# Kernel tuning notes

Hardware: AMD Instinct MI355X
Metric: run time of the kernel (lower is better)

The kernel has to match this reference:

```python
import jax, jax.numpy as jnp
import numpy as np

N_E, E_DIM, BETA = 1024, 64, 0.25

def setup_inputs() -> dict:
    key = jax.random.key(0)
    k1, k2 = jax.random.split(key)
    z = jax.random.normal(k1, (16, 4096, E_DIM), dtype=jnp.float32)
    embedding = jax.random.uniform(k2, (N_E, E_DIM), dtype=jnp.float32,
                                   minval=-1.0 / 256, maxval=1.0 / 256)
    return {"z": z, "embedding": embedding}

def reference(z, embedding):
    # z: [B, S, D]; embedding: [n_e, D]
    zf = z.reshape(-1, E_DIM)  # [N, D]
    # squared euclidean distances: ||z||^2 + ||e||^2 - 2 z e^T -> [N, n_e]
    d = (jnp.sum(zf * zf, axis=1, keepdims=True)
         + jnp.sum(embedding * embedding, axis=1)
         - 2.0 * jnp.matmul(zf, embedding.T))
    min_encoding_indices = jnp.argmin(d, axis=1)  # [N]
    z_q = embedding[min_encoding_indices].reshape(z.shape)  # [B, S, D]
    sg = jax.lax.stop_gradient
    loss = (jnp.mean((z_q - sg(z)) ** 2)
            + BETA * jnp.mean((sg(z_q) - z) ** 2))
    z_q = z + sg(z_q - z)  # straight-through estimator
    return (loss, z_q, min_encoding_indices)
```

## Files before the change

kernel.cpp:

```cpp
#include <hip/hip_runtime.h>


#define D 64
#define NE 1024
#define ROWS 64
#define TCODES 64
#define NTILES 16
#define TPB 256
#define ZSTR 64

#define SWZ(row, c) (((row) << 6) + ((((c) ^ ((row) & 7))) << 2))

__global__ __launch_bounds__(64, 4) void ee_kernel(const float* __restrict__ emb,
                                                   float* __restrict__ ee_ws) {
    const int j = blockIdx.x * 64 + threadIdx.x;
    {
#pragma clang fp contract(off)
        const float4* e4 = (const float4*)(emb + ((size_t)j << 6));
        float4 a = e4[0], b = e4[1];
        float r[8];
        r[0]=a.x*a.x; r[1]=a.y*a.y; r[2]=a.z*a.z; r[3]=a.w*a.w;
        r[4]=b.x*b.x; r[5]=b.y*b.y; r[6]=b.z*b.z; r[7]=b.w*b.w;
#pragma unroll
        for (int g = 1; g < 8; ++g) {
            float4 c = e4[2*g], e = e4[2*g + 1];
            r[0]=r[0]+c.x*c.x; r[1]=r[1]+c.y*c.y;
            r[2]=r[2]+c.z*c.z; r[3]=r[3]+c.w*c.w;
            r[4]=r[4]+e.x*e.x; r[5]=r[5]+e.y*e.y;
            r[6]=r[6]+e.z*e.z; r[7]=r[7]+e.w*e.w;
        }
        ee_ws[j] = ((r[0]+r[1])+(r[2]+r[3])) + ((r[4]+r[5])+(r[6]+r[7]));
    }
}

__global__ __launch_bounds__(TPB, 3) void vq_kernel(const float* __restrict__ z,
                                                    const float* __restrict__ emb,
                                                    const float* __restrict__ ee_ws,
                                                    float* __restrict__ out_loss,
                                                    float* __restrict__ out_zq,
                                                    float* __restrict__ out_idx,
                                                    float loss_scale) {
    __shared__ __align__(16) float z_lds[ROWS * ZSTR];
    __shared__ __align__(16) float e_lds[TCODES * ZSTR];
    __shared__ float ee_lds[NE];
    __shared__ float zz_lds[ROWS];
    __shared__ float smv[2 * ROWS];
    __shared__ int   smi[2 * ROWS];

    const int tid  = threadIdx.x;
    const int lane = tid & 63;
    const int w    = tid >> 6;
    const int rh   = w & 1;
    const int ch   = w >> 1;
    const int i8   = lane & 7;
    const int jg   = lane >> 3;
    const size_t blockRow = (size_t)blockIdx.x * ROWS;
    const int zrow0 = (rh << 5) + i8;

    {
        const float4* zg4 = (const float4*)(z + blockRow * D);
#pragma unroll
        for (int it = 0; it < 4; ++it) {
            int idx = tid + it * TPB;
            float4 v = zg4[idx];
            *(float4*)&z_lds[SWZ(idx >> 4, idx & 15)] = v;
        }
    }
    {
        float4 v = ((const float4*)ee_ws)[tid];
        *(float4*)&ee_lds[tid * 4] = v;
    }
    float4 pe0, pe1, pe2, pe3;
    {
        const float4* eg4 = (const float4*)emb;
        pe0 = eg4[tid];       pe1 = eg4[tid + 256];
        pe2 = eg4[tid + 512]; pe3 = eg4[tid + 768];
    }
    __syncthreads();

    if (tid < ROWS) {
        float zr[D];
#pragma unroll
        for (int c = 0; c < 16; ++c) {
            float4 v = *(const float4*)&z_lds[SWZ(tid, c)];
            zr[4*c+0]=v.x; zr[4*c+1]=v.y; zr[4*c+2]=v.z; zr[4*c+3]=v.w;
        }
        {
#pragma clang fp contract(off)
            float r[8];
#pragma unroll
            for (int jj = 0; jj < 8; ++jj) { float t = zr[jj]*zr[jj]; r[jj] = t; }
#pragma unroll
            for (int i = 8; i < 64; i += 8) {
#pragma unroll
                for (int jj = 0; jj < 8; ++jj) { float t = zr[i+jj]*zr[i+jj]; r[jj] = r[jj] + t; }
            }
            zz_lds[tid] = ((r[0]+r[1])+(r[2]+r[3])) + ((r[4]+r[5])+(r[6]+r[7]));
        }
    }

    float rb[4];  int rbj[4];
#pragma unroll
    for (int rr = 0; rr < 4; ++rr) { rb[rr] = __builtin_inff(); rbj[rr] = 0; }

    for (int t = 0; t < NTILES; ++t) {
        *(float4*)&e_lds[SWZ((tid      ) >> 4, (tid      ) & 15)] = pe0;
        *(float4*)&e_lds[SWZ((tid + 256) >> 4, (tid + 256) & 15)] = pe1;
        *(float4*)&e_lds[SWZ((tid + 512) >> 4, (tid + 512) & 15)] = pe2;
        *(float4*)&e_lds[SWZ((tid + 768) >> 4, (tid + 768) & 15)] = pe3;
        __syncthreads();

        if (t < NTILES - 1) {
            const float4* eg4 = (const float4*)(emb + (size_t)(t + 1) * TCODES * D);
            pe0 = eg4[tid];       pe1 = eg4[tid + 256];
            pe2 = eg4[tid + 512]; pe3 = eg4[tid + 768];
        }

        float4 acc[4][4];
#pragma unroll
        for (int rr = 0; rr < 4; ++rr)
#pragma unroll
            for (int cc = 0; cc < 4; ++cc)
                acc[rr][cc] = make_float4(0.f, 0.f, 0.f, 0.f);

#pragma unroll 2
        for (int c = 0; c < 16; ++c) {
            float4 zf[4], ef[4];
#pragma unroll
            for (int rr = 0; rr < 4; ++rr)
                zf[rr] = *(const float4*)&z_lds[SWZ(zrow0 + 8*rr, c)];
#pragma unroll
            for (int cc = 0; cc < 4; ++cc)
                ef[cc] = *(const float4*)&e_lds[SWZ((ch << 5) + jg + (cc << 3), c)];
#pragma unroll
            for (int rr = 0; rr < 4; ++rr)
#pragma unroll
                for (int cc = 0; cc < 4; ++cc) {
                    acc[rr][cc].x = fmaf(zf[rr].x, ef[cc].x, acc[rr][cc].x);
                    acc[rr][cc].y = fmaf(zf[rr].y, ef[cc].y, acc[rr][cc].y);
                    acc[rr][cc].z = fmaf(zf[rr].z, ef[cc].z, acc[rr][cc].z);
                    acc[rr][cc].w = fmaf(zf[rr].w, ef[cc].w, acc[rr][cc].w);
                }
        }

        const int cbase = t * TCODES + (ch << 5) + jg;
        const float ee0 = ee_lds[cbase];
        const float ee1 = ee_lds[cbase + 8];
        const float ee2 = ee_lds[cbase + 16];
        const float ee3 = ee_lds[cbase + 24];
#pragma unroll
        for (int rr = 0; rr < 4; ++rr) {
            const float zzv = zz_lds[zrow0 + 8*rr];
            float dot0 = (acc[rr][0].x + acc[rr][0].y) + (acc[rr][0].z + acc[rr][0].w);
            float dot1 = (acc[rr][1].x + acc[rr][1].y) + (acc[rr][1].z + acc[rr][1].w);
            float dot2 = (acc[rr][2].x + acc[rr][2].y) + (acc[rr][2].z + acc[rr][2].w);
            float dot3 = (acc[rr][3].x + acc[rr][3].y) + (acc[rr][3].z + acc[rr][3].w);
            float d0 = fmaf(-2.0f, dot0, zzv + ee0);
            float d1 = fmaf(-2.0f, dot1, zzv + ee1);
            float d2 = fmaf(-2.0f, dot2, zzv + ee2);
            float d3 = fmaf(-2.0f, dot3, zzv + ee3);
            float cv = d0; int cj = cbase;
            if (d1 < cv) { cv = d1; cj = cbase + 8;  }
            if (d2 < cv) { cv = d2; cj = cbase + 16; }
            if (d3 < cv) { cv = d3; cj = cbase + 24; }
            if (cv < rb[rr]) { rb[rr] = cv; rbj[rr] = cj; }
        }
        __syncthreads();
    }

#pragma unroll
    for (int rr = 0; rr < 4; ++rr) {
        float bv = rb[rr]; int bj = rbj[rr];
#pragma unroll
        for (int off = 8; off <= 32; off <<= 1) {
            float ov = __shfl_xor(bv, off);
            int   oi = __shfl_xor(bj, off);
            if (ov < bv || (ov == bv && oi < bj)) { bv = ov; bj = oi; }
        }
        if (jg == 0) {
            smv[ch * ROWS + zrow0 + 8*rr] = bv;
            smi[ch * ROWS + zrow0 + 8*rr] = bj;
        }
    }
    __syncthreads();

    const int erow = tid & 63;
    const int eg   = tid >> 6;

    float best = smv[erow]; int bi = smi[erow];
    {
        float v  = smv[ROWS + erow];
        int   ii = smi[ROWS + erow];
        if (v < best || (v == best && ii < bi)) { best = v; bi = ii; }
    }

    const float4* qe4 = (const float4*)(emb + ((size_t)bi << 6));
    float s = 0.f;
    float* orow = out_zq + (blockRow + erow) * D;
#pragma unroll
    for (int c = 0; c < 16; ++c) {
        float4 q  = qe4[c];
        float4 zv = *(const float4*)&z_lds[SWZ(erow, c)];
        float d0 = q.x - zv.x, d1 = q.y - zv.y, d2 = q.z - zv.z, d3 = q.w - zv.w;
        s += d0*d0; s += d1*d1; s += d2*d2; s += d3*d3;
        if ((c >> 2) == eg) {
            orow[4*c+0] = zv.x + d0; orow[4*c+1] = zv.y + d1;
            orow[4*c+2] = zv.z + d2; orow[4*c+3] = zv.w + d3;
        }
    }

    if (eg == 0) {
        out_idx[blockRow + erow] = (float)bi;
#pragma unroll
        for (int off = 32; off; off >>= 1) s += __shfl_down(s, off);
        if (tid == 0) atomicAdd(out_loss, s * loss_scale);
    }
}

extern "C" void kernel_launch(void* const* d_in, const int* in_sizes, int n_in,
                              void* d_out, int out_size, void* d_ws, size_t ws_size,
                              hipStream_t stream) {
    const float* z   = (const float*)d_in[0];
    const float* emb = (const float*)d_in[1];
    const int nz = in_sizes[0];
    const int N  = nz / D;

    float* out      = (float*)d_out;
    float* out_zq   = out + 1;
    float* out_idx  = out + 1 + (size_t)nz;
    float* ee_ws    = (float*)d_ws;

    const float loss_scale = 1.25f / (float)nz;

    hipMemsetAsync(out, 0, sizeof(float), stream);
    ee_kernel<<<NE / 64, 64, 0, stream>>>(emb, ee_ws);
    vq_kernel<<<N / ROWS, TPB, 0, stream>>>(z, emb, ee_ws, out, out_zq, out_idx,
                                            loss_scale);
}
```

Measured before the change: 217.0 us.

## Double codebook tile to 128 codes and give each wave all 64 rows

Codebook tiles grow from 64 to 128 codes, so the tile loop runs 8 times instead of 16 with half as many barriers. Each wave now covers all 64 z rows against its own 32 codes, so per-thread accumulators go from 16 to 32 float4 and every loaded code vector is reused across twice as many rows. The cross-wave argmin reduction widens from 2 to 4 partials. The cost is much higher register pressure (launch bounds lowered to 2 blocks per CU), a larger LDS footprint and twice the prefetch registers, all of which reduce occupancy.

```diff
diff --git a/kernel.cpp b/kernel.cpp
--- a/kernel.cpp
+++ b/kernel.cpp
@@ -4,8 +4,8 @@
 #define D 64
 #define NE 1024
 #define ROWS 64
-#define TCODES 64
-#define NTILES 16
+#define TCODES 128
+#define NTILES 8
 #define TPB 256
 #define ZSTR 64
 
@@ -33,7 +33,7 @@
     }
 }
 
-__global__ __launch_bounds__(TPB, 3) void vq_kernel(const float* __restrict__ z,
+__global__ __launch_bounds__(TPB, 2) void vq_kernel(const float* __restrict__ z,
                                                     const float* __restrict__ emb,
                                                     const float* __restrict__ ee_ws,
                                                     float* __restrict__ out_loss,
@@ -44,18 +44,15 @@
     __shared__ __align__(16) float e_lds[TCODES * ZSTR];
     __shared__ float ee_lds[NE];
     __shared__ float zz_lds[ROWS];
-    __shared__ float smv[2 * ROWS];
-    __shared__ int   smi[2 * ROWS];
+    __shared__ float smv[4 * ROWS];
+    __shared__ int   smi[4 * ROWS];
 
     const int tid  = threadIdx.x;
     const int lane = tid & 63;
     const int w    = tid >> 6;
-    const int rh   = w & 1;
-    const int ch   = w >> 1;
     const int i8   = lane & 7;
     const int jg   = lane >> 3;
     const size_t blockRow = (size_t)blockIdx.x * ROWS;
-    const int zrow0 = (rh << 5) + i8;
 
     {
         const float4* zg4 = (const float4*)(z + blockRow * D);
@@ -70,11 +67,13 @@
         float4 v = ((const float4*)ee_ws)[tid];
         *(float4*)&ee_lds[tid * 4] = v;
     }
-    float4 pe0, pe1, pe2, pe3;
+    float4 pe0, pe1, pe2, pe3, pe4, pe5, pe6, pe7;
     {
         const float4* eg4 = (const float4*)emb;
-        pe0 = eg4[tid];       pe1 = eg4[tid + 256];
-        pe2 = eg4[tid + 512]; pe3 = eg4[tid + 768];
+        pe0 = eg4[tid];        pe1 = eg4[tid + 256];
+        pe2 = eg4[tid + 512];  pe3 = eg4[tid + 768];
+        pe4 = eg4[tid + 1024]; pe5 = eg4[tid + 1280];
+        pe6 = eg4[tid + 1536]; pe7 = eg4[tid + 1792];
     }
     __syncthreads();
 
@@ -99,41 +98,47 @@
         }
     }
 
-    float rb[4];  int rbj[4];
-#pragma unroll
-    for (int rr = 0; rr < 4; ++rr) { rb[rr] = __builtin_inff(); rbj[rr] = 0; }
+    float rb[8];  int rbj[8];
+#pragma unroll
+    for (int rr = 0; rr < 8; ++rr) { rb[rr] = __builtin_inff(); rbj[rr] = 0; }
 
     for (int t = 0; t < NTILES; ++t) {
-        *(float4*)&e_lds[SWZ((tid      ) >> 4, (tid      ) & 15)] = pe0;
-        *(float4*)&e_lds[SWZ((tid + 256) >> 4, (tid + 256) & 15)] = pe1;
-        *(float4*)&e_lds[SWZ((tid + 512) >> 4, (tid + 512) & 15)] = pe2;
-        *(float4*)&e_lds[SWZ((tid + 768) >> 4, (tid + 768) & 15)] = pe3;
+        *(float4*)&e_lds[SWZ((tid       ) >> 4, (tid       ) & 15)] = pe0;
+        *(float4*)&e_lds[SWZ((tid +  256) >> 4, (tid +  256) & 15)] = pe1;
+        *(float4*)&e_lds[SWZ((tid +  512) >> 4, (tid +  512) & 15)] = pe2;
+        *(float4*)&e_lds[SWZ((tid +  768) >> 4, (tid +  768) & 15)] = pe3;
+        *(float4*)&e_lds[SWZ((tid + 1024) >> 4, (tid + 1024) & 15)] = pe4;
+        *(float4*)&e_lds[SWZ((tid + 1280) >> 4, (tid + 1280) & 15)] = pe5;
+        *(float4*)&e_lds[SWZ((tid + 1536) >> 4, (tid + 1536) & 15)] = pe6;
+        *(float4*)&e_lds[SWZ((tid + 1792) >> 4, (tid + 1792) & 15)] = pe7;
         __syncthreads();
 
         if (t < NTILES - 1) {
             const float4* eg4 = (const float4*)(emb + (size_t)(t + 1) * TCODES * D);
-            pe0 = eg4[tid];       pe1 = eg4[tid + 256];
-            pe2 = eg4[tid + 512]; pe3 = eg4[tid + 768];
-        }
-
-        float4 acc[4][4];
-#pragma unroll
-        for (int rr = 0; rr < 4; ++rr)
+            pe0 = eg4[tid];        pe1 = eg4[tid + 256];
+            pe2 = eg4[tid + 512];  pe3 = eg4[tid + 768];
+            pe4 = eg4[tid + 1024]; pe5 = eg4[tid + 1280];
+            pe6 = eg4[tid + 1536]; pe7 = eg4[tid + 1792];
+        }
+
+        float4 acc[8][4];
+#pragma unroll
+        for (int rr = 0; rr < 8; ++rr)
 #pragma unroll
             for (int cc = 0; cc < 4; ++cc)
                 acc[rr][cc] = make_float4(0.f, 0.f, 0.f, 0.f);
 
 #pragma unroll 2
         for (int c = 0; c < 16; ++c) {
-            float4 zf[4], ef[4];
-#pragma unroll
-            for (int rr = 0; rr < 4; ++rr)
-                zf[rr] = *(const float4*)&z_lds[SWZ(zrow0 + 8*rr, c)];
+            float4 zf[8], ef[4];
+#pragma unroll
+            for (int rr = 0; rr < 8; ++rr)
+                zf[rr] = *(const float4*)&z_lds[SWZ(i8 + 8*rr, c)];
 #pragma unroll
             for (int cc = 0; cc < 4; ++cc)
-                ef[cc] = *(const float4*)&e_lds[SWZ((ch << 5) + jg + (cc << 3), c)];
-#pragma unroll
-            for (int rr = 0; rr < 4; ++rr)
+                ef[cc] = *(const float4*)&e_lds[SWZ((w << 5) + jg + (cc << 3), c)];
+#pragma unroll
+            for (int rr = 0; rr < 8; ++rr)
 #pragma unroll
                 for (int cc = 0; cc < 4; ++cc) {
                     acc[rr][cc].x = fmaf(zf[rr].x, ef[cc].x, acc[rr][cc].x);
@@ -143,14 +148,14 @@
                 }
         }
 
-        const int cbase = t * TCODES + (ch << 5) + jg;
+        const int cbase = t * TCODES + (w << 5) + jg;
         const float ee0 = ee_lds[cbase];
         const float ee1 = ee_lds[cbase + 8];
         const float ee2 = ee_lds[cbase + 16];
         const float ee3 = ee_lds[cbase + 24];
 #pragma unroll
-        for (int rr = 0; rr < 4; ++rr) {
-            const float zzv = zz_lds[zrow0 + 8*rr];
+        for (int rr = 0; rr < 8; ++rr) {
+            const float zzv = zz_lds[i8 + 8*rr];
             float dot0 = (acc[rr][0].x + acc[rr][0].y) + (acc[rr][0].z + acc[rr][0].w);
             float dot1 = (acc[rr][1].x + acc[rr][1].y) + (acc[rr][1].z + acc[rr][1].w);
             float dot2 = (acc[rr][2].x + acc[rr][2].y) + (acc[rr][2].z + acc[rr][2].w);
@@ -169,7 +174,7 @@
     }
 
 #pragma unroll
-    for (int rr = 0; rr < 4; ++rr) {
+    for (int rr = 0; rr < 8; ++rr) {
         float bv = rb[rr]; int bj = rbj[rr];
 #pragma unroll
         for (int off = 8; off <= 32; off <<= 1) {
@@ -178,8 +183,8 @@
             if (ov < bv || (ov == bv && oi < bj)) { bv = ov; bj = oi; }
         }
         if (jg == 0) {
-            smv[ch * ROWS + zrow0 + 8*rr] = bv;
-            smi[ch * ROWS + zrow0 + 8*rr] = bj;
+            smv[w * ROWS + i8 + 8*rr] = bv;
+            smi[w * ROWS + i8 + 8*rr] = bj;
         }
     }
     __syncthreads();
@@ -188,9 +193,10 @@
     const int eg   = tid >> 6;
 
     float best = smv[erow]; int bi = smi[erow];
-    {
-        float v  = smv[ROWS + erow];
-        int   ii = smi[ROWS + erow];
+#pragma unroll
+    for (int s2 = 1; s2 < 4; ++s2) {
+        float v  = smv[s2 * ROWS + erow];
+        int   ii = smi[s2 * ROWS + erow];
         if (v < best || (v == best && ii < bi)) { best = v; bi = ii; }
     }
 
```

New measurement: 212.6 us. 2.0% less time.
